# Kernel tuning notes

Measured on AMD Instinct MI355X. Metric: run time of the kernel, lower is better.

## Reference

```python
import jax, jax.numpy as jnp
import numpy as np

K = 0.001  # sigmoid temperature from DGCLoss init
EPS = 1e-8


def _off_diag(m):
    # [..., n, n] -> [..., n, n-1], removing the diagonal in row-major order
    n = m.shape[-1]
    lead = m.shape[:-2]
    flat = m.reshape(lead + (n * n,))[..., :-1]
    return flat.reshape(lead + (n - 1, n + 1))[..., 1:].reshape(lead + (n, n - 1))


def setup_inputs() -> dict:
    key = jax.random.key(0)
    k1, k2 = jax.random.split(key)
    ranking = jax.random.normal(k1, (384, 256), dtype=jnp.float32)
    gt = jax.random.randint(k2, (384,), 0, 6, dtype=jnp.int64)
    return {"ranking": ranking, "gt": gt}


def reference(ranking, gt):
    x = ranking
    N = x.shape[0]
    # cosine similarity matrix, mapped to [0, 1]
    xn = x / jnp.clip(jnp.linalg.norm(x, axis=1, keepdims=True), EPS, None)
    sm = (xn @ xn.T + 1.0) * 0.5                         # [N, N]
    rank = _off_diag(sm)                                 # [N, N-1]
    g = jnp.abs(gt[None, :] - gt[:, None]).astype(jnp.float32)  # [N, N]
    g = _off_diag(g)                                     # [N, N-1]
    M = N - 1
    # dij[n, i, j] = rank[n, j] - rank[n, i]
    dij = rank[:, None, :] - rank[:, :, None]            # [N, M, M]
    dij = _off_diag(dij)                                 # [N, M, M-1]
    # clamped sigmoid indicator
    indicator = 1.0 / (1.0 + jnp.exp(jnp.clip(-dij / K, -50.0, 50.0)))
    indicator = indicator.sum(-1) + 1.0                  # [N, M]
    relevance = jnp.exp2(jnp.clip(10.0 - g, 0.0, None)) - 1.0  # [N, M]
    dcg = (relevance / jnp.log2(indicator + 1.0)).sum(axis=1)  # [N]
    # ideal DCG from sorted relevance
    rel_sorted = jnp.sort(relevance, axis=-1)[:, ::-1]
    discount = jnp.log2(jnp.arange(M, dtype=jnp.float32) + 2.0)
    idcg = (rel_sorted / discount).sum(axis=-1)          # [N]
    valid = idcg != 0.0
    ndcg = jnp.where(valid, dcg / jnp.where(valid, idcg, 1.0), 0.0)
    cnt = valid.sum()
    mean_ndcg = ndcg.sum() / jnp.maximum(cnt, 1).astype(jnp.float32)
    return jnp.where(cnt == 0, jnp.float32(1.0), 1.0 - mean_ndcg)
```

## Files before the change

kernel.cpp:

```cpp
#include <hip/hip_runtime.h>


#define NN 384
#define DD 256
#define MM 383
#define HSCALE 721.3475204444817f
#define NBUCK  256
#define BSCALE 0.1767955801104972f
#define WWIN   6.0f

__global__ __launch_bounds__(256) void dgc_trans(const float* __restrict__ x,
                                                 float* __restrict__ XT,
                                                 float* __restrict__ invn_g) {
    __shared__ float xs[16][260];
    __shared__ float invn[16];
    const int t  = threadIdx.x;
    const int r0 = blockIdx.x * 16;

    #pragma unroll
    for (int i = 0; i < 4; ++i) {
        int f = t + i * 256;
        int r = f >> 6, c4 = f & 63;
        float4 v = ((const float4*)(x + (size_t)(r0 + r) * DD))[c4];
        xs[r][c4 * 4 + 0] = v.x; xs[r][c4 * 4 + 1] = v.y;
        xs[r][c4 * 4 + 2] = v.z; xs[r][c4 * 4 + 3] = v.w;
    }
    __syncthreads();

    {
        const int r = t >> 4, sub = t & 15;
        float s = 0.0f;
        #pragma unroll
        for (int m = 0; m < 16; ++m) {
            float v = xs[r][sub * 16 + m];
            s = fmaf(v, v, s);
        }
        #pragma unroll
        for (int off = 8; off > 0; off >>= 1) s += __shfl_xor(s, off, 64);
        if (sub == 0) invn[r] = __builtin_amdgcn_rsqf(fmaxf(s, 1e-16f));
    }
    __syncthreads();

    if (t < 16) invn_g[r0 + t] = invn[t];

    {
        const int r  = t & 15;
        const int kk = t >> 4;
        const float inv = invn[r];
        #pragma unroll
        for (int i = 0; i < 16; ++i) {
            int k = i * 16 + kk;
            XT[(size_t)k * NN + r0 + r] = xs[r][k] * inv;
        }
    }
}

__global__ __launch_bounds__(768) void dgc_fused(const float* __restrict__ XT,
                                                 const float* __restrict__ x,
                                                 const float* __restrict__ invn_g,
                                                 const int* __restrict__ gt,
                                                 float* __restrict__ ndcg) {
    __shared__ float  xs[2][DD];
    __shared__ float4 pacc[2][8][96];
    __shared__ float  srow[2][NN];
    __shared__ float  vsort[2][NN];
    __shared__ int    sidx[2][NN];
    __shared__ int    hist[2][NBUCK];
    __shared__ int    pre[2][NBUCK + 1];
    __shared__ int    cnt[6];
    __shared__ int    cum[2][6];
    __shared__ float  redd[12];
    __shared__ float  idr[12][2];

    const int n0   = blockIdx.x * 2;
    const int t    = threadIdx.x;
    const int lane = t & 63;
    const int wave = t >> 6;

    if (t < 128) {
        const int rr = t >> 6;
        const float inv = invn_g[n0 + rr];
        float4 v = ((const float4*)(x + (size_t)(n0 + rr) * DD))[t & 63];
        v.x *= inv; v.y *= inv; v.z *= inv; v.w *= inv;
        ((float4*)xs[rr])[t & 63] = v;
    }
    if (t < 512) ((int*)hist)[t] = 0;
    if (t < 6)  cnt[t] = 0;
    if (t < 24) ((float*)idr)[t] = 0.0f;
    __syncthreads();

    if (t < NN) atomicAdd(&cnt[gt[t]], 1);

    {
        const int j4 = t % 96;
        const int kc = t / 96;
        const float4* XT4 = (const float4*)XT;
        float4 a0 = {0.f, 0.f, 0.f, 0.f};
        float4 a1 = {0.f, 0.f, 0.f, 0.f};
        const int k0 = kc * 32;
        #pragma unroll 8
        for (int m = 0; m < 32; ++m) {
            const int k = k0 + m;
            float4 b = XT4[(size_t)k * 96 + j4];
            float s0 = xs[0][k];
            float s1 = xs[1][k];
            a0.x = fmaf(s0, b.x, a0.x); a0.y = fmaf(s0, b.y, a0.y);
            a0.z = fmaf(s0, b.z, a0.z); a0.w = fmaf(s0, b.w, a0.w);
            a1.x = fmaf(s1, b.x, a1.x); a1.y = fmaf(s1, b.y, a1.y);
            a1.z = fmaf(s1, b.z, a1.z); a1.w = fmaf(s1, b.w, a1.w);
        }
        pacc[0][kc][j4] = a0;
        pacc[1][kc][j4] = a1;
    }
    __syncthreads();

    const int r = t / 384;
    const int u = t - r * 384;

    if (t < 2) {
        const int gv = gt[n0 + t];
        int h[6];
        #pragma unroll
        for (int g = 0; g < 6; ++g) h[g] = 0;
        #pragma unroll
        for (int v = 0; v < 6; ++v) {
            int d = v - gv; d = d < 0 ? -d : d;
            h[d] += cnt[v];
        }
        h[0] -= 1;
        int s = 0;
        #pragma unroll
        for (int g = 0; g < 6; ++g) { s += h[g]; cum[t][g] = s; }
    }

    {
        const float* pf = (const float*)pacc[r];
        float dot = 0.0f;
        #pragma unroll
        for (int c = 0; c < 8; ++c) dot += pf[c * 384 + u];
        srow[r][u] = fmaf(dot, HSCALE, HSCALE);
    }
    __syncthreads();

    const float vraw = srow[r][u];
    int b = (int)(vraw * BSCALE);
    b = b < 0 ? 0 : (b > NBUCK - 1 ? NBUCK - 1 : b);
    const int slot = atomicAdd(&hist[r][b], 1);
    __syncthreads();

    if (wave == 0 || wave == 6) {
        const int rr = wave / 6;
        const int s0 = hist[rr][lane * 4 + 0], s1 = hist[rr][lane * 4 + 1];
        const int s2 = hist[rr][lane * 4 + 2], s3 = hist[rr][lane * 4 + 3];
        const int sum = s0 + s1 + s2 + s3;
        int inc = sum;
        #pragma unroll
        for (int off = 1; off < 64; off <<= 1) {
            int uu = __shfl_up(inc, off, 64);
            if (lane >= off) inc += uu;
        }
        const int base = inc - sum;
        pre[rr][lane * 4 + 0] = base;
        pre[rr][lane * 4 + 1] = base + s0;
        pre[rr][lane * 4 + 2] = base + s0 + s1;
        pre[rr][lane * 4 + 3] = base + s0 + s1 + s2;
        if (lane == 63) pre[rr][NBUCK] = inc;
    } else {
        const int p = (wave < 6) ? (wave - 1) * 64 + lane
                                 : 320 + (wave - 7) * 64 + lane;
        float a0 = 0.0f, a1 = 0.0f;
        if (p < MM) {
            const float invl = 1.0f / __builtin_amdgcn_logf((float)(p + 2));
            const int g0 = (p >= cum[0][0]) + (p >= cum[0][1]) + (p >= cum[0][2])
                         + (p >= cum[0][3]) + (p >= cum[0][4]);
            const int g1 = (p >= cum[1][0]) + (p >= cum[1][1]) + (p >= cum[1][2])
                         + (p >= cum[1][3]) + (p >= cum[1][4]);
            a0 = (float)((1 << (10 - g0)) - 1) * invl;
            a1 = (float)((1 << (10 - g1)) - 1) * invl;
        }
        #pragma unroll
        for (int off = 32; off > 0; off >>= 1) {
            a0 += __shfl_down(a0, off, 64);
            a1 += __shfl_down(a1, off, 64);
        }
        if (lane == 0) { idr[wave][0] = a0; idr[wave][1] = a1; }
    }
    __syncthreads();

    {
        const int pos = pre[r][b] + slot;
        vsort[r][pos] = vraw;
        sidx[r][pos]  = u;
    }
    __syncthreads();

    const int   nrow  = n0 + r;
    const float ri    = vsort[r][u];
    const int   iorig = sidx[r][u];
    const float sn    = srow[r][nrow];

    int Blo = (int)((ri - WWIN) * BSCALE);
    int Bhi = (int)((ri + WWIN) * BSCALE);
    Blo = Blo < 0 ? 0 : (Blo > NBUCK - 1 ? NBUCK - 1 : Blo);
    Bhi = Bhi < 0 ? 0 : (Bhi > NBUCK - 1 ? NBUCK - 1 : Bhi);
    const int lo = pre[r][Blo];
    const int hi = pre[r][Bhi + 1];

    float acc = 0.0f;
    int q = lo;
    for (; q + 2 <= hi; q += 2) {
        float a  = __builtin_amdgcn_exp2f(ri - vsort[r][q]);
        float bb = __builtin_amdgcn_exp2f(ri - vsort[r][q + 1]);
        float e = a + bb;
        float f = a * bb;
        acc = fmaf(2.0f + e, __builtin_amdgcn_rcpf(1.0f + e + f), acc);
    }
    if (q < hi)
        acc += __builtin_amdgcn_rcpf(1.0f + __builtin_amdgcn_exp2f(ri - vsort[r][q]));
    float sum_all = (float)(NN - hi) + acc;

    int bn = (int)(sn * BSCALE);
    bn = bn < 0 ? 0 : (bn > NBUCK - 1 ? NBUCK - 1 : bn);
    float cd = 0.0f;
    if (bn > Bhi)       cd = 1.0f;
    else if (bn >= Blo) cd = __builtin_amdgcn_rcpf(1.0f + __builtin_amdgcn_exp2f(ri - sn));
    const float ind = 0.5f + sum_all - cd;

    float dcg_i = 0.0f;
    if (iorig != nrow) {
        const int gd = gt[iorig] - gt[nrow];
        const int gg = gd < 0 ? -gd : gd;
        dcg_i = (float)((1 << (10 - gg)) - 1) / __builtin_amdgcn_logf(ind + 1.0f);
    }

    #pragma unroll
    for (int off = 32; off > 0; off >>= 1) dcg_i += __shfl_down(dcg_i, off, 64);
    if (lane == 0) redd[wave] = dcg_i;
    __syncthreads();

    if (t == 0) {
        const float id = idr[1][0] + idr[2][0] + idr[3][0] + idr[4][0] + idr[5][0]
                       + idr[7][0] + idr[8][0] + idr[9][0] + idr[10][0] + idr[11][0];
        ndcg[n0] = (redd[0] + redd[1] + redd[2] + redd[3] + redd[4] + redd[5]) / id;
    }
    if (t == 384) {
        const float id = idr[1][1] + idr[2][1] + idr[3][1] + idr[4][1] + idr[5][1]
                       + idr[7][1] + idr[8][1] + idr[9][1] + idr[10][1] + idr[11][1];
        ndcg[n0 + 1] = (redd[6] + redd[7] + redd[8] + redd[9] + redd[10] + redd[11])
                       / id;
    }
}

__global__ __launch_bounds__(384) void dgc_final(const float* __restrict__ ndcg,
                                                 float* __restrict__ out) {
    __shared__ float red[6];
    const int t    = threadIdx.x;
    const int lane = t & 63;
    const int wave = t >> 6;
    float nd = ndcg[t];
    #pragma unroll
    for (int off = 32; off > 0; off >>= 1) nd += __shfl_down(nd, off, 64);
    if (lane == 0) red[wave] = nd;
    __syncthreads();
    if (t == 0) {
        float s = 0.0f;
        for (int w = 0; w < 6; ++w) s += red[w];
        out[0] = 1.0f - s / (float)NN;
    }
}

extern "C" void kernel_launch(void* const* d_in, const int* in_sizes, int n_in,
                              void* d_out, int out_size, void* d_ws, size_t ws_size,
                              hipStream_t stream) {
    const float* ranking = (const float*)d_in[0];
    const int*   gt      = (const int*)d_in[1];
    float*       out     = (float*)d_out;

    float* XT     = (float*)d_ws;
    float* invn_g = XT + (size_t)DD * NN;
    float* ndcg   = invn_g + NN;

    dgc_trans<<<24, 256, 0, stream>>>(ranking, XT, invn_g);
    dgc_fused<<<NN / 2, 768, 0, stream>>>(XT, ranking, invn_g, gt, ndcg);
    dgc_final<<<1, 384, 0, stream>>>(ndcg, out);
}
```

Before: 69.81 us.

## Fuse transpose, main and final kernels into one cooperative kernel

Merges the normalize/transpose kernel, the main NDCG kernel and the final reduction into a single cooperative launch. Grid-wide syncs replace the kernel boundaries between stages. The aim is to remove the launch gaps between three kernels. In exchange it adds two grid barriers, extra shared memory per block, and a requirement that all 192 blocks be resident at the same time.

New measurement: 121.0 us. 73.4% more time.

```diff
diff --git a/kernel.cpp b/kernel.cpp
--- a/kernel.cpp
+++ b/kernel.cpp
@@ -1,4 +1,7 @@
 #include <hip/hip_runtime.h>
+#include <hip/hip_cooperative_groups.h>
+
+namespace cg = cooperative_groups;
 
 
 #define NN 384
@@ -9,57 +12,14 @@
 #define BSCALE 0.1767955801104972f
 #define WWIN   6.0f
 
-__global__ __launch_bounds__(256) void dgc_trans(const float* __restrict__ x,
-                                                 float* __restrict__ XT,
-                                                 float* __restrict__ invn_g) {
-    __shared__ float xs[16][260];
-    __shared__ float invn[16];
-    const int t  = threadIdx.x;
-    const int r0 = blockIdx.x * 16;
-
-    #pragma unroll
-    for (int i = 0; i < 4; ++i) {
-        int f = t + i * 256;
-        int r = f >> 6, c4 = f & 63;
-        float4 v = ((const float4*)(x + (size_t)(r0 + r) * DD))[c4];
-        xs[r][c4 * 4 + 0] = v.x; xs[r][c4 * 4 + 1] = v.y;
-        xs[r][c4 * 4 + 2] = v.z; xs[r][c4 * 4 + 3] = v.w;
-    }
-    __syncthreads();
-
-    {
-        const int r = t >> 4, sub = t & 15;
-        float s = 0.0f;
-        #pragma unroll
-        for (int m = 0; m < 16; ++m) {
-            float v = xs[r][sub * 16 + m];
-            s = fmaf(v, v, s);
-        }
-        #pragma unroll
-        for (int off = 8; off > 0; off >>= 1) s += __shfl_xor(s, off, 64);
-        if (sub == 0) invn[r] = __builtin_amdgcn_rsqf(fmaxf(s, 1e-16f));
-    }
-    __syncthreads();
-
-    if (t < 16) invn_g[r0 + t] = invn[t];
-
-    {
-        const int r  = t & 15;
-        const int kk = t >> 4;
-        const float inv = invn[r];
-        #pragma unroll
-        for (int i = 0; i < 16; ++i) {
-            int k = i * 16 + kk;
-            XT[(size_t)k * NN + r0 + r] = xs[r][k] * inv;
-        }
-    }
-}
-
-__global__ __launch_bounds__(768) void dgc_fused(const float* __restrict__ XT,
-                                                 const float* __restrict__ x,
-                                                 const float* __restrict__ invn_g,
-                                                 const int* __restrict__ gt,
-                                                 float* __restrict__ ndcg) {
+__global__ __launch_bounds__(768) void dgc_all(const float* __restrict__ x,
+                                               const int* __restrict__ gt,
+                                               float* __restrict__ XT,
+                                               float* __restrict__ invn_g,
+                                               float* __restrict__ ndcg,
+                                               float* __restrict__ out) {
+    __shared__ float xs_t[16][260];
+    __shared__ float invn_s[16];
     __shared__ float  xs[2][DD];
     __shared__ float4 pacc[2][8][96];
     __shared__ float  srow[2][NN];
@@ -72,10 +32,49 @@
     __shared__ float  redd[12];
     __shared__ float  idr[12][2];
 
-    const int n0   = blockIdx.x * 2;
+    cg::grid_group grid = cg::this_grid();
+
     const int t    = threadIdx.x;
     const int lane = t & 63;
     const int wave = t >> 6;
+
+    if (blockIdx.x < 24) {
+        const int r0 = blockIdx.x * 16;
+        for (int f = t; f < 1024; f += 768) {
+            int rr = f >> 6, c4 = f & 63;
+            float4 v = ((const float4*)(x + (size_t)(r0 + rr) * DD))[c4];
+            xs_t[rr][c4 * 4 + 0] = v.x; xs_t[rr][c4 * 4 + 1] = v.y;
+            xs_t[rr][c4 * 4 + 2] = v.z; xs_t[rr][c4 * 4 + 3] = v.w;
+        }
+        __syncthreads();
+        if (t < 256) {
+            const int rr = t >> 4, sub = t & 15;
+            float s = 0.0f;
+            #pragma unroll
+            for (int m = 0; m < 16; ++m) {
+                float v = xs_t[rr][sub * 16 + m];
+                s = fmaf(v, v, s);
+            }
+            #pragma unroll
+            for (int off = 8; off > 0; off >>= 1) s += __shfl_xor(s, off, 64);
+            if (sub == 0) invn_s[rr] = __builtin_amdgcn_rsqf(fmaxf(s, 1e-16f));
+        }
+        __syncthreads();
+        if (t < 16) invn_g[r0 + t] = invn_s[t];
+        if (t < 256) {
+            const int rr = t & 15;
+            const int kk = t >> 4;
+            const float inv = invn_s[rr];
+            #pragma unroll
+            for (int i = 0; i < 16; ++i) {
+                int k = i * 16 + kk;
+                XT[(size_t)k * NN + r0 + rr] = xs_t[rr][k] * inv;
+            }
+        }
+    }
+    grid.sync();
+
+    const int n0 = blockIdx.x * 2;
 
     if (t < 128) {
         const int rr = t >> 6;
@@ -249,23 +248,21 @@
         ndcg[n0 + 1] = (redd[6] + redd[7] + redd[8] + redd[9] + redd[10] + redd[11])
                        / id;
     }
-}
-
-__global__ __launch_bounds__(384) void dgc_final(const float* __restrict__ ndcg,
-                                                 float* __restrict__ out) {
-    __shared__ float red[6];
-    const int t    = threadIdx.x;
-    const int lane = t & 63;
-    const int wave = t >> 6;
-    float nd = ndcg[t];
-    #pragma unroll
-    for (int off = 32; off > 0; off >>= 1) nd += __shfl_down(nd, off, 64);
-    if (lane == 0) red[wave] = nd;
-    __syncthreads();
-    if (t == 0) {
-        float s = 0.0f;
-        for (int w = 0; w < 6; ++w) s += red[w];
-        out[0] = 1.0f - s / (float)NN;
+
+    grid.sync();
+
+    if (blockIdx.x == 0) {
+        float nd = (t < NN) ? ndcg[t] : 0.0f;
+        #pragma unroll
+        for (int off = 32; off > 0; off >>= 1) nd += __shfl_down(nd, off, 64);
+        if (lane == 0) redd[wave] = nd;
+        __syncthreads();
+        if (t == 0) {
+            float s = 0.0f;
+            #pragma unroll
+            for (int w = 0; w < 6; ++w) s += redd[w];
+            out[0] = 1.0f - s / (float)NN;
+        }
     }
 }
 
@@ -280,7 +277,8 @@
     float* invn_g = XT + (size_t)DD * NN;
     float* ndcg   = invn_g + NN;
 
-    dgc_trans<<<24, 256, 0, stream>>>(ranking, XT, invn_g);
-    dgc_fused<<<NN / 2, 768, 0, stream>>>(XT, ranking, invn_g, gt, ndcg);
-    dgc_final<<<1, 384, 0, stream>>>(ndcg, out);
+    void* args[] = {(void*)&ranking, (void*)&gt, (void*)&XT,
+                    (void*)&invn_g, (void*)&ndcg, (void*)&out};
+    hipLaunchCooperativeKernel((void*)dgc_all, dim3(NN / 2), dim3(768),
+                               args, 0, stream);
 }
```
